# Optimization experiments

Hardware: AMD Instinct MI355X
Metric: run time of the kernel (lower is better)

The kernel has to match this reference:

```python
import jax, jax.numpy as jnp
import numpy as np

NUM_CAPSULE = 16
DIM_CAPSULE = 32
ROUTINGS = 4
EPS = 1e-07


def squash(x, axis=-1):
    # NOTE: faithful to the source: x / sqrt(sum(x^2) + eps) (unit-norm style),
    # NOT the standard Hinton squash.
    s2 = jnp.sum(x * x, axis=axis, keepdims=True)
    return x / jnp.sqrt(s2 + EPS)


def setup_inputs() -> dict:
    key = jax.random.key(0)
    k1, k2 = jax.random.split(key)
    B, N_in, D_in = 128, 1024, 256
    x = jax.random.normal(k1, (B, N_in, D_in), dtype=jnp.float32)
    # xavier_normal over (1, D_in, NUM_CAPSULE*DIM_CAPSULE)
    fan_in, fan_out = D_in, NUM_CAPSULE * DIM_CAPSULE
    std = np.sqrt(2.0 / (fan_in + fan_out))
    W = jax.random.normal(k2, (1, D_in, NUM_CAPSULE * DIM_CAPSULE), dtype=jnp.float32) * std
    return {"x": x, "W": W}


def reference(x, W):
    B, N_in, _ = x.shape
    # u_hat: [B, N_in, num_cap*dim_cap] -> [B, num_cap, N_in, dim_cap]
    u_hat = jnp.matmul(x, W[0])
    u_hat = u_hat.reshape(B, N_in, NUM_CAPSULE, DIM_CAPSULE).transpose(0, 2, 1, 3)

    b = jnp.zeros((B, NUM_CAPSULE, N_in), dtype=u_hat.dtype)
    outputs = None
    for i in range(ROUTINGS):
        # torch permutes to softmax over the num_capsule axis; equivalent to axis=1 here
        c = jax.nn.softmax(b, axis=1)                      # [B, num_cap, N_in]
        outputs = squash(jnp.einsum('bij,bijk->bik', c, u_hat))  # [B, num_cap, dim_cap]
        if i < ROUTINGS - 1:
            b = jnp.einsum('bik,bijk->bij', outputs, u_hat)
    return outputs
```

## Files before the change

### kernel.cpp

```cpp
#include <hip/hip_runtime.h>

typedef unsigned int u32;
typedef unsigned short u16;
typedef float f32x4 __attribute__((ext_vector_type(4)));
typedef __bf16 bf16x8 __attribute__((ext_vector_type(8)));

#define BATCH 128
#define NIN   1024
#define DIN   256
#define NC    16
#define DC    32
#define NCOL  512

__device__ __forceinline__ float bflo(u32 v){ return __uint_as_float(v << 16); }
__device__ __forceinline__ float bfhi(u32 v){ return __uint_as_float(v & 0xffff0000u); }
__device__ __forceinline__ u32 bfround(u32 ua){ return (ua + 0x7fffu + ((ua >> 16) & 1u)) >> 16; }
__device__ __forceinline__ u32 pack2(float a, float b){
    return (bfround(__float_as_uint(a)) & 0xffffu) | (bfround(__float_as_uint(b)) << 16);
}

__device__ __forceinline__ int lds_x(int r, int d){
    int sw = (d >> 2) ^ ((r & 7) << 1) ^ (((r >> 3) & 3) << 2);
    return r * 256 + (sw << 2) + (d & 3);
}

__global__ __launch_bounds__(256) void k_pre(const float* __restrict__ x, const float* __restrict__ W,
                                             uint4* __restrict__ xbT, float* __restrict__ s,
                                             uint2* __restrict__ Wb){
    __shared__ __align__(16) u16 xt[64 * 256];
    const int t = threadIdx.x, jc8 = blockIdx.x, b = blockIdx.y;

    if (jc8 == 0){
        float4 w4 = ((const float4*)W)[b * 256 + t];
        Wb[b * 256 + t] = make_uint2(pack2(w4.x, w4.y), pack2(w4.z, w4.w));
    }
    {
        const float4* xg = (const float4*)(x + ((size_t)b * NIN + jc8 * 64) * DIN);
        int d4 = t & 63;
        #pragma unroll
        for (int m = 0; m < 16; m++){
            int r = (t >> 6) + 4 * m;
            float4 v = xg[r * 64 + d4];
            *(uint2*)&xt[lds_x(r, d4 * 4)] = make_uint2(pack2(v.x, v.y), pack2(v.z, v.w));
        }
    }
    __syncthreads();
    {
        float acc = 0.f;
        #pragma unroll
        for (int r = 0; r < 64; r++) acc += bflo((u32)xt[lds_x(r, t)]);
        atomicAdd(&s[b * DIN + t], acc);
    }
    #pragma unroll
    for (int w = 0; w < 8; w++){
        int oid = t + 256 * w;
        int lane = oid & 63, js2 = (oid >> 6) & 1, dt = oid >> 7;
        int l15 = lane & 15, q = lane >> 4;
        int rb = js2 * 32 + q * 8, d = dt * 16 + l15;
        u32 r[4];
        #pragma unroll
        for (int p = 0; p < 4; p++){
            u32 lo = xt[lds_x(rb + 2 * p, d)];
            u32 hi = xt[lds_x(rb + 2 * p + 1, d)];
            r[p] = lo | (hi << 16);
        }
        xbT[(((size_t)b * 16 + dt) * 32 + (jc8 * 2 + js2)) * 64 + lane] = make_uint4(r[0], r[1], r[2], r[3]);
    }
}

__global__ __launch_bounds__(256) void k_main(const float* __restrict__ x, const uint4* __restrict__ xbT,
                                              const u16* __restrict__ vb, float* __restrict__ zp){
    __shared__ float bbl[16][132];
    __shared__ __align__(16) u16 cl[16][136];
    const int t = threadIdx.x, jh = blockIdx.x, b = blockIdx.y;
    const int lane = t & 63, wv = t >> 6;
    const int l15 = lane & 15, q = lane >> 4;

    uint4 vfrag[8];
    #pragma unroll
    for (int ks = 0; ks < 8; ks++)
        vfrag[ks] = *(const uint4*)&vb[((size_t)b * 16 + l15) * 256 + ks * 32 + q * 8];

    #pragma unroll
    for (int u = 0; u < 2; u++){
        int jt = wv * 2 + u;
        const float* xr = x + ((size_t)b * NIN + jh * 128 + jt * 16 + l15) * DIN + q * 8;
        float4 xa[8][2];
        #pragma unroll
        for (int ks = 0; ks < 8; ks++){
            xa[ks][0] = *(const float4*)(xr + ks * 32);
            xa[ks][1] = *(const float4*)(xr + ks * 32 + 4);
        }
        f32x4 acc = {0.f, 0.f, 0.f, 0.f};
        #pragma unroll
        for (int ks = 0; ks < 8; ks++){
            uint4 xw;
            xw.x = pack2(xa[ks][0].x, xa[ks][0].y);
            xw.y = pack2(xa[ks][0].z, xa[ks][0].w);
            xw.z = pack2(xa[ks][1].x, xa[ks][1].y);
            xw.w = pack2(xa[ks][1].z, xa[ks][1].w);
            acc = __builtin_amdgcn_mfma_f32_16x16x32_bf16(
                __builtin_bit_cast(bf16x8, vfrag[ks]), __builtin_bit_cast(bf16x8, xw), acc, 0, 0, 0);
        }
        #pragma unroll
        for (int r = 0; r < 4; r++) bbl[q * 4 + r][jt * 16 + l15] = acc[r];
    }
    __syncthreads();

    if (t < 128){
        float mx = -1e30f, e[16], sum = 0.f;
        #pragma unroll
        for (int i = 0; i < 16; i++) mx = fmaxf(mx, bbl[i][t]);
        #pragma unroll
        for (int i = 0; i < 16; i++){ e[i] = __expf(bbl[i][t] - mx); sum += e[i]; }
        float inv = 1.f / sum;
        #pragma unroll
        for (int i = 0; i < 16; i++) cl[i][t] = (u16)bfround(__float_as_uint(e[i] * inv));
    }
    __syncthreads();

    bf16x8 cfrag[4];
    #pragma unroll
    for (int ksj = 0; ksj < 4; ksj++)
        cfrag[ksj] = __builtin_bit_cast(bf16x8, *(const uint4*)&cl[l15][ksj * 32 + q * 8]);
    #pragma unroll
    for (int u = 0; u < 4; u++){
        int dt = wv * 4 + u;
        f32x4 acc = {0.f, 0.f, 0.f, 0.f};
        #pragma unroll
        for (int ksj = 0; ksj < 4; ksj++){
            uint4 bw = xbT[(((size_t)b * 16 + dt) * 32 + jh * 4 + ksj) * 64 + lane];
            acc = __builtin_amdgcn_mfma_f32_16x16x32_bf16(
                cfrag[ksj], __builtin_bit_cast(bf16x8, bw), acc, 0, 0, 0);
        }
        float* zpb = zp + ((((size_t)jh * 128 + b) * 16) * 256) + dt * 16 + l15;
        #pragma unroll
        for (int r = 0; r < 4; r++) zpb[(size_t)(q * 4 + r) * 256] = acc[r];
    }
}

__global__ __launch_bounds__(512) void k_tail(const float* __restrict__ s, const float* __restrict__ zp,
                                              const u16* __restrict__ Wb, u16* __restrict__ vb,
                                              float* __restrict__ out, int mode){
    __shared__ float zl[16][260];
    __shared__ __align__(16) float ol[512];
    const int b = blockIdx.x, t = threadIdx.x;
    const int i = t >> 5;
    float y = 0.f;
    if (mode == 0){
        if (t < 256) zl[0][t] = s[b * 256 + t] * (1.f / 16.f);
        __syncthreads();
        #pragma unroll 8
        for (int d = 0; d < 256; d++) y += zl[0][d] * bflo((u32)Wb[d * 512 + t]);
    } else {
        #pragma unroll
        for (int u0 = 0; u0 < 8; u0++){
            int idx = t + 512 * u0;
            int ii = idx >> 8, dd = idx & 255;
            float acc = 0.f;
            #pragma unroll
            for (int jh = 0; jh < 8; jh++)
                acc += zp[((((size_t)jh * 128 + b) * 16 + ii) * 256) + dd];
            zl[ii][dd] = acc;
        }
        __syncthreads();
        #pragma unroll 8
        for (int d = 0; d < 256; d++) y += zl[i][d] * bflo((u32)Wb[d * 512 + t]);
    }
    float s2 = y * y;
    s2 += __shfl_xor(s2, 1); s2 += __shfl_xor(s2, 2); s2 += __shfl_xor(s2, 4);
    s2 += __shfl_xor(s2, 8); s2 += __shfl_xor(s2, 16);
    float r = y / sqrtf(s2 + 1e-7f);
    if (mode == 2){ out[b * 512 + t] = r; return; }
    ol[t] = r;
    __syncthreads();
    {
        int d = t & 255, ih = t >> 8;
        #pragma unroll
        for (int ii2 = 0; ii2 < 8; ii2++){
            int i2 = ih * 8 + ii2;
            const float4* op = (const float4*)&ol[i2 * 32];
            float acc = 0.f;
            #pragma unroll
            for (int w4 = 0; w4 < 4; w4++){
                uint4 wv4 = *(const uint4*)&Wb[(size_t)d * 512 + i2 * 32 + w4 * 8];
                float4 o0 = op[w4 * 2], o1 = op[w4 * 2 + 1];
                acc += o0.x * bflo(wv4.x) + o0.y * bfhi(wv4.x) + o0.z * bflo(wv4.y) + o0.w * bfhi(wv4.y)
                     + o1.x * bflo(wv4.z) + o1.y * bfhi(wv4.z) + o1.z * bflo(wv4.w) + o1.w * bfhi(wv4.w);
            }
            vb[((size_t)b * 16 + i2) * 256 + d] = (u16)bfround(__float_as_uint(acc));
        }
    }
}

extern "C" void kernel_launch(void* const* d_in, const int* in_sizes, int n_in,
                              void* d_out, int out_size, void* d_ws, size_t ws_size,
                              hipStream_t stream){
    const float* x = (const float*)d_in[0];
    const float* W = (const float*)d_in[1];
    float* out = (float*)d_out;
    char* ws = (char*)d_ws;
    float* s    = (float*)(ws);
    u16*   vb   = (u16*)  (ws + 131072);
    u16*   Wb   = (u16*)  (ws + 1179648);
    float* zp   = (float*)(ws + 1441792);
    uint4* xbT  = (uint4*)(ws + 18219008);

    hipMemsetAsync(s, 0, 131072, stream);
    k_pre<<<dim3(16, BATCH), 256, 0, stream>>>(x, W, xbT, s, (uint2*)Wb);
    k_tail<<<BATCH, 512, 0, stream>>>(s, zp, Wb, vb, out, 0);
    for (int it = 1; it < 4; it++){
        k_main<<<dim3(8, BATCH), 256, 0, stream>>>(x, xbT, vb, zp);
        k_tail<<<BATCH, 512, 0, stream>>>(s, zp, Wb, vb, out, it == 3 ? 2 : 1);
    }
}
```

Baseline: 371.8 us.

## Cache bf16 copy of x for routing passes and split tail kernel per batch

```diff
diff --git a/kernel.cpp b/kernel.cpp
--- a/kernel.cpp
+++ b/kernel.cpp
@@ -18,6 +18,9 @@
 __device__ __forceinline__ u32 pack2(float a, float b){
     return (bfround(__float_as_uint(a)) & 0xffffu) | (bfround(__float_as_uint(b)) << 16);
 }
+__device__ __forceinline__ bf16x8 ldfrag(const u16* p){
+    return __builtin_bit_cast(bf16x8, *(const uint4*)p);
+}
 
 __device__ __forceinline__ int lds_x(int r, int d){
     int sw = (d >> 2) ^ ((r & 7) << 1) ^ (((r >> 3) & 3) << 2);
@@ -25,23 +28,34 @@
 }
 
 __global__ __launch_bounds__(256) void k_pre(const float* __restrict__ x, const float* __restrict__ W,
-                                             uint4* __restrict__ xbT, float* __restrict__ s,
-                                             uint2* __restrict__ Wb){
+                                             uint4* __restrict__ xbT, u16* __restrict__ xb,
+                                             float* __restrict__ s, uint2* __restrict__ Wb,
+                                             uint2* __restrict__ WT){
     __shared__ __align__(16) u16 xt[64 * 256];
     const int t = threadIdx.x, jc8 = blockIdx.x, b = blockIdx.y;
 
     if (jc8 == 0){
-        float4 w4 = ((const float4*)W)[b * 256 + t];
-        Wb[b * 256 + t] = make_uint2(pack2(w4.x, w4.y), pack2(w4.z, w4.w));
+        int id = b * 256 + t;
+        float4 w4 = ((const float4*)W)[id];
+        Wb[id] = make_uint2(pack2(w4.x, w4.y), pack2(w4.z, w4.w));
+        int c = id >> 6, d4 = id & 63;
+        float e0 = W[(size_t)(d4 * 4 + 0) * NCOL + c];
+        float e1 = W[(size_t)(d4 * 4 + 1) * NCOL + c];
+        float e2 = W[(size_t)(d4 * 4 + 2) * NCOL + c];
+        float e3 = W[(size_t)(d4 * 4 + 3) * NCOL + c];
+        WT[c * 64 + d4] = make_uint2(pack2(e0, e1), pack2(e2, e3));
     }
     {
         const float4* xg = (const float4*)(x + ((size_t)b * NIN + jc8 * 64) * DIN);
+        uint2* xbw = (uint2*)xb + ((size_t)(b * NIN + jc8 * 64)) * 64;
         int d4 = t & 63;
         #pragma unroll
         for (int m = 0; m < 16; m++){
             int r = (t >> 6) + 4 * m;
             float4 v = xg[r * 64 + d4];
-            *(uint2*)&xt[lds_x(r, d4 * 4)] = make_uint2(pack2(v.x, v.y), pack2(v.z, v.w));
+            uint2 p = make_uint2(pack2(v.x, v.y), pack2(v.z, v.w));
+            *(uint2*)&xt[lds_x(r, d4 * 4)] = p;
+            xbw[r * 64 + d4] = p;
         }
     }
     __syncthreads();
@@ -68,7 +82,7 @@
     }
 }
 
-__global__ __launch_bounds__(256) void k_main(const float* __restrict__ x, const uint4* __restrict__ xbT,
+__global__ __launch_bounds__(256) void k_main(const u16* __restrict__ xb, const uint4* __restrict__ xbT,
                                               const u16* __restrict__ vb, float* __restrict__ zp){
     __shared__ float bbl[16][132];
     __shared__ __align__(16) u16 cl[16][136];
@@ -81,27 +95,16 @@
     for (int ks = 0; ks < 8; ks++)
         vfrag[ks] = *(const uint4*)&vb[((size_t)b * 16 + l15) * 256 + ks * 32 + q * 8];
 
+    const u16* xrow = xb + ((size_t)(b * NIN + jh * 128)) * 256;
     #pragma unroll
     for (int u = 0; u < 2; u++){
         int jt = wv * 2 + u;
-        const float* xr = x + ((size_t)b * NIN + jh * 128 + jt * 16 + l15) * DIN + q * 8;
-        float4 xa[8][2];
-        #pragma unroll
-        for (int ks = 0; ks < 8; ks++){
-            xa[ks][0] = *(const float4*)(xr + ks * 32);
-            xa[ks][1] = *(const float4*)(xr + ks * 32 + 4);
-        }
+        const u16* xr = xrow + (jt * 16 + l15) * 256 + q * 8;
         f32x4 acc = {0.f, 0.f, 0.f, 0.f};
         #pragma unroll
-        for (int ks = 0; ks < 8; ks++){
-            uint4 xw;
-            xw.x = pack2(xa[ks][0].x, xa[ks][0].y);
-            xw.y = pack2(xa[ks][0].z, xa[ks][0].w);
-            xw.z = pack2(xa[ks][1].x, xa[ks][1].y);
-            xw.w = pack2(xa[ks][1].z, xa[ks][1].w);
+        for (int ks = 0; ks < 8; ks++)
             acc = __builtin_amdgcn_mfma_f32_16x16x32_bf16(
-                __builtin_bit_cast(bf16x8, vfrag[ks]), __builtin_bit_cast(bf16x8, xw), acc, 0, 0, 0);
-        }
+                __builtin_bit_cast(bf16x8, vfrag[ks]), ldfrag(xr + ks * 32), acc, 0, 0, 0);
         #pragma unroll
         for (int r = 0; r < 4; r++) bbl[q * 4 + r][jt * 16 + l15] = acc[r];
     }
@@ -139,56 +142,57 @@
     }
 }
 
-__global__ __launch_bounds__(512) void k_tail(const float* __restrict__ s, const float* __restrict__ zp,
-                                              const u16* __restrict__ Wb, u16* __restrict__ vb,
-                                              float* __restrict__ out, int mode){
-    __shared__ float zl[16][260];
-    __shared__ __align__(16) float ol[512];
-    const int b = blockIdx.x, t = threadIdx.x;
-    const int i = t >> 5;
+__global__ __launch_bounds__(256) void k_tail(const float* __restrict__ s, const float* __restrict__ zp,
+                                              const u16* __restrict__ Wb, const u32* __restrict__ WT32,
+                                              u16* __restrict__ vb, float* __restrict__ out, int mode){
+    __shared__ float zl[8][260];
+    __shared__ __align__(16) float ol[256];
+    const int ih2 = blockIdx.x, b = blockIdx.y, t = threadIdx.x;
+    const int i_loc = t >> 5;
+    const int o_idx = ih2 * 256 + t;
     float y = 0.f;
     if (mode == 0){
-        if (t < 256) zl[0][t] = s[b * 256 + t] * (1.f / 16.f);
+        zl[0][t] = s[b * 256 + t] * (1.f / 16.f);
         __syncthreads();
         #pragma unroll 8
-        for (int d = 0; d < 256; d++) y += zl[0][d] * bflo((u32)Wb[d * 512 + t]);
+        for (int d = 0; d < 256; d++) y += zl[0][d] * bflo((u32)Wb[d * 512 + o_idx]);
     } else {
         #pragma unroll
         for (int u0 = 0; u0 < 8; u0++){
-            int idx = t + 512 * u0;
+            int idx = t + 256 * u0;
             int ii = idx >> 8, dd = idx & 255;
+            int ig = ih2 * 8 + ii;
             float acc = 0.f;
             #pragma unroll
             for (int jh = 0; jh < 8; jh++)
-                acc += zp[((((size_t)jh * 128 + b) * 16 + ii) * 256) + dd];
+                acc += zp[((((size_t)jh * 128 + b) * 16 + ig) * 256) + dd];
             zl[ii][dd] = acc;
         }
         __syncthreads();
         #pragma unroll 8
-        for (int d = 0; d < 256; d++) y += zl[i][d] * bflo((u32)Wb[d * 512 + t]);
+        for (int d = 0; d < 256; d++) y += zl[i_loc][d] * bflo((u32)Wb[d * 512 + o_idx]);
     }
     float s2 = y * y;
     s2 += __shfl_xor(s2, 1); s2 += __shfl_xor(s2, 2); s2 += __shfl_xor(s2, 4);
     s2 += __shfl_xor(s2, 8); s2 += __shfl_xor(s2, 16);
     float r = y / sqrtf(s2 + 1e-7f);
-    if (mode == 2){ out[b * 512 + t] = r; return; }
+    if (mode == 2){ out[b * 512 + o_idx] = r; return; }
     ol[t] = r;
     __syncthreads();
     {
-        int d = t & 255, ih = t >> 8;
-        #pragma unroll
-        for (int ii2 = 0; ii2 < 8; ii2++){
-            int i2 = ih * 8 + ii2;
-            const float4* op = (const float4*)&ol[i2 * 32];
-            float acc = 0.f;
+        int dh = t & 127, ihalf = t >> 7;
+        #pragma unroll
+        for (int e = 0; e < 4; e++){
+            int ii = ihalf * 4 + e;
+            int i2 = ih2 * 8 + ii;
+            float a0 = 0.f, a1 = 0.f;
             #pragma unroll
-            for (int w4 = 0; w4 < 4; w4++){
-                uint4 wv4 = *(const uint4*)&Wb[(size_t)d * 512 + i2 * 32 + w4 * 8];
-                float4 o0 = op[w4 * 2], o1 = op[w4 * 2 + 1];
-                acc += o0.x * bflo(wv4.x) + o0.y * bfhi(wv4.x) + o0.z * bflo(wv4.y) + o0.w * bfhi(wv4.y)
-                     + o1.x * bflo(wv4.z) + o1.y * bfhi(wv4.z) + o1.z * bflo(wv4.w) + o1.w * bfhi(wv4.w);
+            for (int k = 0; k < 32; k++){
+                u32 wv2 = WT32[(size_t)(i2 * 32 + k) * 128 + dh];
+                float ok = ol[ii * 32 + k];
+                a0 += ok * bflo(wv2); a1 += ok * bfhi(wv2);
             }
-            vb[((size_t)b * 16 + i2) * 256 + d] = (u16)bfround(__float_as_uint(acc));
+            ((u32*)vb)[(size_t)(b * 16 + i2) * 128 + dh] = pack2(a0, a1);
         }
     }
 }
@@ -203,14 +207,16 @@
     float* s    = (float*)(ws);
     u16*   vb   = (u16*)  (ws + 131072);
     u16*   Wb   = (u16*)  (ws + 1179648);
-    float* zp   = (float*)(ws + 1441792);
-    uint4* xbT  = (uint4*)(ws + 18219008);
+    u32*   WT   = (u32*)  (ws + 1441792);
+    float* zp   = (float*)(ws + 1703936);
+    u16*   xb   = (u16*)  (ws + 18481152);
+    uint4* xbT  = (uint4*)(ws + 85590016);
 
     hipMemsetAsync(s, 0, 131072, stream);
-    k_pre<<<dim3(16, BATCH), 256, 0, stream>>>(x, W, xbT, s, (uint2*)Wb);
-    k_tail<<<BATCH, 512, 0, stream>>>(s, zp, Wb, vb, out, 0);
+    k_pre<<<dim3(16, BATCH), 256, 0, stream>>>(x, W, xbT, xb, s, (uint2*)Wb, (uint2*)WT);
+    k_tail<<<dim3(2, BATCH), 256, 0, stream>>>(s, zp, Wb, WT, vb, out, 0);
     for (int it = 1; it < 4; it++){
-        k_main<<<dim3(8, BATCH), 256, 0, stream>>>(x, xbT, vb, zp);
-        k_tail<<<BATCH, 512, 0, stream>>>(s, zp, Wb, vb, out, it == 3 ? 2 : 1);
-    }
-}
+        k_main<<<dim3(8, BATCH), 256, 0, stream>>>(xb, xbT, vb, zp);
+        k_tail<<<dim3(2, BATCH), 256, 0, stream>>>(s, zp, Wb, WT, vb, out, it == 3 ? 2 : 1);
+    }
+}
```

Result: faster. 361.9 us (-2.7%).
